# Optimization experiments

Hardware: AMD Instinct MI355X
Metric: run time of the kernel (lower is better)

The kernel has to match this reference:

```python
import jax, jax.numpy as jnp
import numpy as np

B, S, D_IN, D_EMB = 8, 2048, 512, 512

def setup_inputs() -> dict:
    key = jax.random.key(0)
    ks = jax.random.split(key, 7)
    s = 1.0 / np.sqrt(D_IN)
    return {
        "x": jax.random.normal(ks[0], (B, S, D_IN), dtype=jnp.float32),
        "Wq": jax.random.uniform(ks[1], (D_IN, D_EMB), jnp.float32, -s, s),
        "bq": jax.random.uniform(ks[2], (D_EMB,), jnp.float32, -s, s),
        "Wk": jax.random.uniform(ks[3], (D_IN, D_EMB), jnp.float32, -s, s),
        "bk": jax.random.uniform(ks[4], (D_EMB,), jnp.float32, -s, s),
        "Wv": jax.random.uniform(ks[5], (D_IN, D_EMB), jnp.float32, -s, s),
        "bv": jax.random.uniform(ks[6], (D_EMB,), jnp.float32, -s, s),
    }

def reference(x, Wq, bq, Wk, bk, Wv, bv):
    # single-head attention: softmax(QK^T / sqrt(d)) V
    q = x @ Wq + bq            # [B,S,E]
    k = x @ Wk + bk
    v = x @ Wv + bv
    scores = jnp.einsum('bse,bte->bst', q, k) / jnp.sqrt(jnp.float32(D_EMB))
    attn = jax.nn.softmax(scores, axis=-1)  # [B,S,S]
    return jnp.einsum('bst,bte->bse', attn, v)
```

## Files before the change

### kernel.cpp

```cpp
#include <hip/hip_runtime.h>
#include <stdint.h>


using f32x4 = __attribute__((ext_vector_type(4))) float;
using s16x8 = __attribute__((ext_vector_type(8))) short;
using u16x4 = __attribute__((ext_vector_type(4))) unsigned short;

#define S_LEN 2048
#define EMB   512

#define ASYNC16(g, l)                                                     \
  __builtin_amdgcn_global_load_lds(                                       \
      (const __attribute__((address_space(1))) void*)(g),                 \
      (__attribute__((address_space(3))) void*)(l), 16, 0, 0)

__device__ __forceinline__ unsigned short f2bf(float f) {
  union { float f; unsigned u; } v; v.f = f;
  unsigned r = v.u + 0x7fffu + ((v.u >> 16) & 1u);
  return (unsigned short)(r >> 16);
}

__global__ __launch_bounds__(256) void xconv_kernel(
    const float* __restrict__ x, short* __restrict__ xb) {
  int i = (blockIdx.x * 256 + threadIdx.x) * 8;
  f32x4 a = *(const f32x4*)(x + i);
  f32x4 b = *(const f32x4*)(x + i + 4);
  s16x8 h;
  h[0] = (short)f2bf(a[0]); h[1] = (short)f2bf(a[1]);
  h[2] = (short)f2bf(a[2]); h[3] = (short)f2bf(a[3]);
  h[4] = (short)f2bf(b[0]); h[5] = (short)f2bf(b[1]);
  h[6] = (short)f2bf(b[2]); h[7] = (short)f2bf(b[3]);
  *(s16x8*)(xb + i) = h;
}

__global__ __launch_bounds__(256) void wconv_kernel(
    const float* __restrict__ Wq, const float* __restrict__ Wk,
    const float* __restrict__ Wv, short* __restrict__ Wt) {
  int idx = blockIdx.x * 256 + threadIdx.x;
  int mat = idx >> 18;
  int r   = idx & 262143;
  int n   = r >> 9;
  int k   = r & 511;
  const float* W = (mat == 0) ? Wq : (mat == 1) ? Wk : Wv;
  Wt[idx] = (short)f2bf(W[k * 512 + n]);
}

__global__ __launch_bounds__(256) void qkv_gemm(
    const short* __restrict__ xb, const short* __restrict__ Wt,
    const float* __restrict__ bq, const float* __restrict__ bk,
    const float* __restrict__ bv,
    short* __restrict__ Qg, short* __restrict__ Kg, short* __restrict__ VTg) {
  __shared__ __align__(16) short As[128 * 64];
  __shared__ __align__(16) short Bs[128 * 64];
  int gid = blockIdx.x;
  int mat = gid >> 9;
  int rem = gid & 511;
  int mt  = rem & 127, nt = rem >> 7;
  int m0  = mt << 7,   n0 = nt << 7;
  const short* W    = Wt + (size_t)mat * 262144;
  const float* bias = (mat == 0) ? bq : (mat == 1) ? bk : bv;

  int tid = threadIdx.x, lane = tid & 63, wv = tid >> 6;
  int l16 = lane & 15, quad = lane >> 4;
  int wr = (wv & 1) << 6, wc = (wv >> 1) << 6;
  int drow = lane >> 3;
  int dchk = (lane & 7) ^ drow;

  const f32x4 Z4 = {0.f, 0.f, 0.f, 0.f};
  f32x4 acc[4][4];
#pragma unroll
  for (int a = 0; a < 4; ++a)
#pragma unroll
    for (int c = 0; c < 4; ++c) acc[a][c] = Z4;

  for (int it = 0; it < 8; ++it) {
    int k0 = it << 6;
    __syncthreads();
#pragma unroll
    for (int i = 0; i < 4; ++i) {
      int g   = wv * 4 + i;
      int row = g * 8 + drow;
      ASYNC16(xb + (size_t)(m0 + row) * 512 + k0 + dchk * 8, &As[g * 512]);
    }
#pragma unroll
    for (int i = 0; i < 4; ++i) {
      int g   = wv * 4 + i;
      int row = g * 8 + drow;
      ASYNC16(W + (size_t)(n0 + row) * 512 + k0 + dchk * 8, &Bs[g * 512]);
    }
    __syncthreads();
#pragma unroll
    for (int kk = 0; kk < 2; ++kk) {
      s16x8 af[4], bfr[4];
#pragma unroll
      for (int rb = 0; rb < 4; ++rb) {
        int row = wr + rb * 16 + l16;
        int c   = kk * 4 + quad;
        af[rb] = *(const s16x8*)(As + row * 64 + ((c ^ (row & 7)) * 8));
      }
#pragma unroll
      for (int cb = 0; cb < 4; ++cb) {
        int row = wc + cb * 16 + l16;
        int c   = kk * 4 + quad;
        bfr[cb] = *(const s16x8*)(Bs + row * 64 + ((c ^ (row & 7)) * 8));
      }
#pragma unroll
      for (int rb = 0; rb < 4; ++rb)
#pragma unroll
        for (int cb = 0; cb < 4; ++cb)
          acc[rb][cb] = __builtin_amdgcn_mfma_f32_16x16x32_bf16(af[rb], bfr[cb], acc[rb][cb], 0, 0, 0);
    }
  }

  float bsv[4];
#pragma unroll
  for (int cb = 0; cb < 4; ++cb) bsv[cb] = bias[n0 + wc + cb * 16 + l16];

  if (mat < 2) {
    short* D = (mat == 0) ? Qg : Kg;
#pragma unroll
    for (int rb = 0; rb < 4; ++rb)
#pragma unroll
      for (int cb = 0; cb < 4; ++cb)
#pragma unroll
        for (int r = 0; r < 4; ++r) {
          int m = m0 + wr + rb * 16 + quad * 4 + r;
          D[(size_t)m * 512 + n0 + wc + cb * 16 + l16] =
              (short)f2bf(acc[rb][cb][r] + bsv[cb]);
        }
  } else {
#pragma unroll
    for (int rb = 0; rb < 4; ++rb)
#pragma unroll
      for (int cb = 0; cb < 4; ++cb) {
        u16x4 h;
#pragma unroll
        for (int r = 0; r < 4; ++r) h[r] = f2bf(acc[rb][cb][r] + bsv[cb]);
        int m  = m0 + wr + rb * 16 + quad * 4;
        int bb = m >> 11, s = m & 2047;
        int e  = n0 + wc + cb * 16 + l16;
        *(u16x4*)(VTg + ((size_t)bb * 512 + e) * 2048 + s) = h;
      }
  }
}

__global__ __launch_bounds__(256, 2) void attn_kernel(
    const short* __restrict__ Qg, const short* __restrict__ Kg,
    const short* __restrict__ VTg, float* __restrict__ out) {
  __shared__ __align__(16) short Kt[32 * 512];
  __shared__ __align__(16) short Vt[512 * 32];
  __shared__ __align__(16) short Pl[32 * 48];
  __shared__ float l_l[32];
  const float SCL2 = 0.06375871855f;

  int b = blockIdx.x & 7, qt = blockIdx.x >> 3;
  int s0 = qt << 5;
  int tid = threadIdx.x, lane = tid & 63, wv = tid >> 6;
  int l16 = lane & 15, quad = lane >> 4;
  int a = wv & 1, h = wv >> 1;
  int e0 = wv << 7;

  const short* Kb = Kg  + ((size_t)b * S_LEN) * 512;
  const short* Vb = VTg + ((size_t)b * 512) * 2048;

  const short* kdma[8];
#pragma unroll
  for (int i = 0; i < 8; ++i) {
    int r = wv * 8 + i;
    kdma[i] = Kb + (size_t)r * 512 + ((lane ^ (i & 7)) * 8);
  }
  int v_er = lane >> 2;
  const short* vdma[8];
#pragma unroll
  for (int i = 0; i < 8; ++i) {
    int g = wv * 8 + i;
    int e = g * 16 + v_er;
    int vc = (lane & 3) ^ ((e >> 1) & 3);
    vdma[i] = Vb + (size_t)e * 2048 + vc * 8;
  }

#pragma unroll
  for (int i = 0; i < 8; ++i)
    ASYNC16(kdma[i], &Kt[(wv * 8 + i) * 512]);

  const short* qrow = Qg + ((size_t)b * S_LEN + s0 + a * 16 + l16) * 512 + quad * 8;
  s16x8 qf[16];
#pragma unroll
  for (int kk = 0; kk < 16; ++kk) qf[kk] = *(const s16x8*)(qrow + kk * 32);

  const f32x4 Z4 = {0.f, 0.f, 0.f, 0.f};
  f32x4 acc[2][8];
#pragma unroll
  for (int rb = 0; rb < 2; ++rb)
#pragma unroll
    for (int cb = 0; cb < 8; ++cb) acc[rb][cb] = Z4;
  f32x4 lsum = Z4;

  __syncthreads();

  for (int kt = 0; kt < 64; ++kt) {
    int t0 = kt << 5;
#pragma unroll
    for (int i = 0; i < 8; ++i)
      ASYNC16(vdma[i] + t0, &Vt[(wv * 8 + i) * 512]);

    f32x4 s_a = Z4, s_b = Z4;
    int krow = h * 16 + l16;
    const short* kb = &Kt[krow * 512];
    int ksw = (krow & 7);
#pragma unroll
    for (int kk = 0; kk < 8; ++kk) {
      s16x8 kf0 = *(const s16x8*)(kb + (((2 * kk) * 4 + quad) ^ ksw) * 8);
      s_a = __builtin_amdgcn_mfma_f32_16x16x32_bf16(qf[2 * kk], kf0, s_a, 0, 0, 0);
      s16x8 kf1 = *(const s16x8*)(kb + (((2 * kk + 1) * 4 + quad) ^ ksw) * 8);
      s_b = __builtin_amdgcn_mfma_f32_16x16x32_bf16(qf[2 * kk + 1], kf1, s_b, 0, 0, 0);
    }
    f32x4 sv = s_a + s_b;

    unsigned short pb[4];
#pragma unroll
    for (int r = 0; r < 4; ++r) {
      float p = exp2f(sv[r] * SCL2);
      pb[r] = f2bf(p);
      lsum[r] += p;
    }
#pragma unroll
    for (int r = 0; r < 4; ++r)
      Pl[(a * 16 + quad * 4 + r) * 48 + h * 16 + l16] = (short)pb[r];

    __syncthreads();

    if (kt + 1 < 64) {
      size_t adv = (size_t)(kt + 1) * 32 * 512;
#pragma unroll
      for (int i = 0; i < 8; ++i)
        ASYNC16(kdma[i] + adv, &Kt[(wv * 8 + i) * 512]);
    }

    s16x8 pf[2];
#pragma unroll
    for (int rb = 0; rb < 2; ++rb)
      pf[rb] = *(const s16x8*)(Pl + (rb * 16 + l16) * 48 + quad * 8);
#pragma unroll
    for (int cb = 0; cb < 8; ++cb) {
      int e  = e0 + cb * 16 + l16;
      int pc = quad ^ ((e >> 1) & 3);
      s16x8 vf = *(const s16x8*)(Vt + e * 32 + pc * 8);
#pragma unroll
      for (int rb = 0; rb < 2; ++rb)
        acc[rb][cb] = __builtin_amdgcn_mfma_f32_16x16x32_bf16(pf[rb], vf, acc[rb][cb], 0, 0, 0);
    }

    __syncthreads();
  }

#pragma unroll
  for (int r = 0; r < 4; ++r) {
    float v = lsum[r];
    v += __shfl_xor(v, 1);
    v += __shfl_xor(v, 2);
    v += __shfl_xor(v, 4);
    v += __shfl_xor(v, 8);
    lsum[r] = v;
  }
  if (h == 0 && l16 == 0) {
#pragma unroll
    for (int r = 0; r < 4; ++r) l_l[a * 16 + quad * 4 + r] = lsum[r];
  }
  __syncthreads();
  if (h == 1 && l16 == 0) {
#pragma unroll
    for (int r = 0; r < 4; ++r) l_l[a * 16 + quad * 4 + r] += lsum[r];
  }
  __syncthreads();

#pragma unroll
  for (int rb = 0; rb < 2; ++rb) {
    f32x4 lv = *(const f32x4*)(l_l + rb * 16 + quad * 4);
    f32x4 li;
#pragma unroll
    for (int r = 0; r < 4; ++r) li[r] = 1.0f / lv[r];
#pragma unroll
    for (int cb = 0; cb < 8; ++cb)
#pragma unroll
      for (int r = 0; r < 4; ++r)
        out[((size_t)b * S_LEN + s0 + rb * 16 + quad * 4 + r) * 512 + e0 + cb * 16 + l16] =
            acc[rb][cb][r] * li[r];
  }
}

extern "C" void kernel_launch(void* const* d_in, const int* in_sizes, int n_in,
                              void* d_out, int out_size, void* d_ws, size_t ws_size,
                              hipStream_t stream) {
  const float* x  = (const float*)d_in[0];
  const float* Wq = (const float*)d_in[1];
  const float* bq = (const float*)d_in[2];
  const float* Wk = (const float*)d_in[3];
  const float* bk = (const float*)d_in[4];
  const float* Wv = (const float*)d_in[5];
  const float* bv = (const float*)d_in[6];

  short* Wt  = (short*)d_ws;
  short* xb  = (short*)((char*)d_ws + 1572864);
  short* Qg  = xb + (size_t)8388608;
  short* Kg  = Qg + (size_t)8388608;
  short* VTg = Kg + (size_t)8388608;

  xconv_kernel<<<4096, 256, 0, stream>>>(x, xb);
  wconv_kernel<<<3072, 256, 0, stream>>>(Wq, Wk, Wv, Wt);
  qkv_gemm<<<1536, 256, 0, stream>>>(xb, Wt, bq, bk, bv, Qg, Kg, VTg);
  attn_kernel<<<512, 256, 0, stream>>>(Qg, Kg, VTg, (float*)d_out);
}
```

Baseline: 258.4 us.

## Double-buffer K and P tiles, load V directly to registers, drop second barrier

The V tile is no longer staged through LDS. Each wave now loads its V fragments straight from global memory into registers at the top of each iteration. K and the probability tile P are double-buffered in LDS, with K prefetched two tiles ahead, so the trailing __syncthreads per iteration can be removed. The aim is to cut LDS traffic and barrier stalls and to overlap global loads with MFMA work. The cost is more register pressure, since eight vector fragments are held live, and global V loads that each wave issues separately without LDS reuse. The P row stride is also changed from 48 to 40.

```diff
diff --git a/kernel.cpp b/kernel.cpp
--- a/kernel.cpp
+++ b/kernel.cpp
@@ -147,9 +147,8 @@
 __global__ __launch_bounds__(256, 2) void attn_kernel(
     const short* __restrict__ Qg, const short* __restrict__ Kg,
     const short* __restrict__ VTg, float* __restrict__ out) {
-  __shared__ __align__(16) short Kt[32 * 512];
-  __shared__ __align__(16) short Vt[512 * 32];
-  __shared__ __align__(16) short Pl[32 * 48];
+  __shared__ __align__(16) short Kt[2][32 * 512];
+  __shared__ __align__(16) short Pl[2][32 * 40];
   __shared__ float l_l[32];
   const float SCL2 = 0.06375871855f;
 
@@ -169,19 +168,14 @@
     int r = wv * 8 + i;
     kdma[i] = Kb + (size_t)r * 512 + ((lane ^ (i & 7)) * 8);
   }
-  int v_er = lane >> 2;
-  const short* vdma[8];
-#pragma unroll
-  for (int i = 0; i < 8; ++i) {
-    int g = wv * 8 + i;
-    int e = g * 16 + v_er;
-    int vc = (lane & 3) ^ ((e >> 1) & 3);
-    vdma[i] = Vb + (size_t)e * 2048 + vc * 8;
-  }
+  const short* vbase = Vb + (size_t)(e0 + l16) * 2048 + quad * 8;
 
 #pragma unroll
   for (int i = 0; i < 8; ++i)
-    ASYNC16(kdma[i], &Kt[(wv * 8 + i) * 512]);
+    ASYNC16(kdma[i], &Kt[0][(wv * 8 + i) * 512]);
+#pragma unroll
+  for (int i = 0; i < 8; ++i)
+    ASYNC16(kdma[i] + 16384, &Kt[1][(wv * 8 + i) * 512]);
 
   const short* qrow = Qg + ((size_t)b * S_LEN + s0 + a * 16 + l16) * 512 + quad * 8;
   s16x8 qf[16];
@@ -199,15 +193,18 @@
   __syncthreads();
 
   for (int kt = 0; kt < 64; ++kt) {
-    int t0 = kt << 5;
-#pragma unroll
-    for (int i = 0; i < 8; ++i)
-      ASYNC16(vdma[i] + t0, &Vt[(wv * 8 + i) * 512]);
+    int cur = kt & 1;
+    int t0  = kt << 5;
+
+    s16x8 vf[8];
+#pragma unroll
+    for (int cb = 0; cb < 8; ++cb)
+      vf[cb] = *(const s16x8*)(vbase + cb * 32768 + t0);
 
     f32x4 s_a = Z4, s_b = Z4;
     int krow = h * 16 + l16;
-    const short* kb = &Kt[krow * 512];
-    int ksw = (krow & 7);
+    const short* kb = &Kt[cur][krow * 512];
+    int ksw = krow & 7;
 #pragma unroll
     for (int kk = 0; kk < 8; ++kk) {
       s16x8 kf0 = *(const s16x8*)(kb + (((2 * kk) * 4 + quad) ^ ksw) * 8);
@@ -217,41 +214,31 @@
     }
     f32x4 sv = s_a + s_b;
 
-    unsigned short pb[4];
 #pragma unroll
     for (int r = 0; r < 4; ++r) {
       float p = exp2f(sv[r] * SCL2);
-      pb[r] = f2bf(p);
       lsum[r] += p;
-    }
-#pragma unroll
-    for (int r = 0; r < 4; ++r)
-      Pl[(a * 16 + quad * 4 + r) * 48 + h * 16 + l16] = (short)pb[r];
+      Pl[cur][(a * 16 + quad * 4 + r) * 40 + h * 16 + l16] = (short)f2bf(p);
+    }
 
     __syncthreads();
 
-    if (kt + 1 < 64) {
-      size_t adv = (size_t)(kt + 1) * 32 * 512;
+    if (kt + 2 < 64) {
+      size_t adv = (size_t)(kt + 2) * 16384;
 #pragma unroll
       for (int i = 0; i < 8; ++i)
-        ASYNC16(kdma[i] + adv, &Kt[(wv * 8 + i) * 512]);
+        ASYNC16(kdma[i] + adv, &Kt[cur][(wv * 8 + i) * 512]);
     }
 
     s16x8 pf[2];
 #pragma unroll
     for (int rb = 0; rb < 2; ++rb)
-      pf[rb] = *(const s16x8*)(Pl + (rb * 16 + l16) * 48 + quad * 8);
-#pragma unroll
-    for (int cb = 0; cb < 8; ++cb) {
-      int e  = e0 + cb * 16 + l16;
-      int pc = quad ^ ((e >> 1) & 3);
-      s16x8 vf = *(const s16x8*)(Vt + e * 32 + pc * 8);
+      pf[rb] = *(const s16x8*)(&Pl[cur][(rb * 16 + l16) * 40 + quad * 8]);
+#pragma unroll
+    for (int cb = 0; cb < 8; ++cb)
 #pragma unroll
       for (int rb = 0; rb < 2; ++rb)
-        acc[rb][cb] = __builtin_amdgcn_mfma_f32_16x16x32_bf16(pf[rb], vf, acc[rb][cb], 0, 0, 0);
-    }
-
-    __syncthreads();
+        acc[rb][cb] = __builtin_amdgcn_mfma_f32_16x16x32_bf16(pf[rb], vf[cb], acc[rb][cb], 0, 0, 0);
   }
 
 #pragma unroll
```

New measurement: 304.2 us. +17.7%, slower.
